# Kernel optimization log

Hardware: AMD Instinct MI355X
Metric: run time of the kernel (lower is better)

The kernel has to match this reference:

```python
import jax, jax.numpy as jnp
import numpy as np

HEADS = 16
HD = 64
LN_EPS = 1e-5


def swish(x):
    return x * jax.nn.sigmoid(x)


def layer_norm(x):
    mu = jnp.mean(x, axis=-1, keepdims=True)
    var = jnp.var(x, axis=-1, keepdims=True)
    return (x - mu) * jax.lax.rsqrt(var + LN_EPS)


def setup_inputs() -> dict:
    key = jax.random.key(0)
    ks = jax.random.split(key, 5)
    B, L, D = 4, 2048, 1024
    x = jax.random.normal(ks[0], (B, L, D), dtype=jnp.float32)
    W_fc = jax.random.normal(ks[1], (D, HEADS * HD * 3), dtype=jnp.float32) * (1.0 / np.sqrt(D))
    b_fc = jax.random.normal(ks[2], (HEADS * HD * 3,), dtype=jnp.float32) * 0.01
    W_fc2 = jax.random.normal(ks[3], (HEADS * HD, D), dtype=jnp.float32) * (1.0 / np.sqrt(HEADS * HD))
    b_fc2 = jax.random.normal(ks[4], (D,), dtype=jnp.float32) * 0.01
    return {"x": x, "W_fc": W_fc, "b_fc": b_fc, "W_fc2": W_fc2, "b_fc2": b_fc2}


def reference(x, W_fc, b_fc, W_fc2, b_fc2):
    B, L, D = x.shape
    # fused QKV projection with swish activation (dropout is identity in eval)
    qkv = swish(jnp.einsum('bld,de->ble', x, W_fc) + b_fc)
    qkv = qkv.reshape(B, L, HEADS, 3 * HD)
    q, k, v = jnp.split(qkv, 3, axis=-1)  # each [B, L, H, hd]
    # NOTE: original scales by sqrt(length), not sqrt(hd)
    scores = jnp.einsum('bwhd,bmhd->bhwm', q, k) / jnp.sqrt(jnp.float32(L))
    att = jax.nn.softmax(scores, axis=-1)  # [B, H, L, L]
    new_v = jnp.einsum('bhwm,bmhd->bwhd', att, v).reshape(B, L, HEADS * HD)
    m = swish(jnp.einsum('ble,ed->bld', new_v, W_fc2) + b_fc2)
    return layer_norm(x + m)
```

## Files before the change

### kernel.cpp

```cpp
#include <hip/hip_runtime.h>
#include <cstddef>
#include <cstdint>

typedef unsigned short u16;
typedef __attribute__((ext_vector_type(8))) short short8;
typedef __attribute__((ext_vector_type(4))) float floatx4;

#define C1_SCALE 0.031882111f
#define LOG2E    1.4426950408889634f

__device__ __forceinline__ u16 f2bf(float f) {
    union { float f; unsigned int i; } v; v.f = f;
    unsigned int b = v.i;
    b += 0x7FFFu + ((b >> 16) & 1u);
    return (u16)(b >> 16);
}

__device__ __forceinline__ unsigned pk2bf(float lo, float hi) {
#if __has_builtin(__builtin_amdgcn_cvt_pk_bf16_f32)
    auto v = __builtin_amdgcn_cvt_pk_bf16_f32(lo, hi);
    union { decltype(v) b; unsigned u; } c; c.b = v; return c.u;
#else
    return (unsigned)f2bf(lo) | ((unsigned)f2bf(hi) << 16);
#endif
}
__device__ __forceinline__ int4 pack8bf(float4 a, float4 b) {
    union { unsigned u[4]; int4 v; } c;
    c.u[0] = pk2bf(a.x, a.y); c.u[1] = pk2bf(a.z, a.w);
    c.u[2] = pk2bf(b.x, b.y); c.u[3] = pk2bf(b.z, b.w);
    return c.v;
}
__device__ __forceinline__ float fastrcp(float x) {
#if __has_builtin(__builtin_amdgcn_rcpf)
    return __builtin_amdgcn_rcpf(x);
#else
    return 1.0f / x;
#endif
}
__device__ __forceinline__ float swishf(float s) {
    float e = __builtin_amdgcn_exp2f(-s * LOG2E);
    return s * fastrcp(1.0f + e);
}
__device__ __forceinline__ void glds16(const void* g, void* l) {
    __builtin_amdgcn_global_load_lds(
        (const __attribute__((address_space(1))) void*)g,
        (__attribute__((address_space(3))) void*)l, 16, 0, 0);
}

__global__ __launch_bounds__(256) void cast_kernel(
    const float* __restrict__ x, u16* __restrict__ xb)
{
    const size_t i = ((size_t)blockIdx.x * 256 + threadIdx.x) * 8;
    float4 a = *(const float4*)&x[i];
    float4 b = *(const float4*)&x[i + 4];
    *(int4*)&xb[i] = pack8bf(a, b);
}

__global__ __launch_bounds__(256) void transpose_kernel(
    const float* __restrict__ src, u16* __restrict__ dst, int R, int C)
{
    __shared__ u16 t[32][33];
    const int tx = threadIdx.x & 31, ty = threadIdx.x >> 5;
    const int r0 = blockIdx.y * 32, c0 = blockIdx.x * 32;
#pragma unroll
    for (int i = 0; i < 4; ++i)
        t[ty + i * 8][tx] = f2bf(src[(size_t)(r0 + ty + i * 8) * C + c0 + tx]);
    __syncthreads();
#pragma unroll
    for (int i = 0; i < 4; ++i)
        dst[(size_t)(c0 + ty + i * 8) * R + r0 + tx] = t[tx][ty + i * 8];
}

#define GEMM_STAGE(AP, BP, Kdim)                                              \
    {                                                                          \
        _Pragma("unroll")                                                      \
        for (int i = 0; i < 4; ++i) {                                          \
            const int row = i * 32 + (tid >> 3);                               \
            const int gp  = (tid & 7) ^ (row & 7);                             \
            glds16(&AP[(size_t)(row0 + row) * Kdim + k0 + gp * 8],             \
                   &As[i * 32 + wid * 8][0]);                                  \
            glds16(&BP[(size_t)(col0 + row) * Kdim + k0 + gp * 8],             \
                   &Bs[i * 32 + wid * 8][0]);                                  \
        }                                                                      \
    }

#define GEMM_COMPUTE()                                                         \
    {                                                                          \
        _Pragma("unroll")                                                      \
        for (int kc = 0; kc < 2; ++kc) {                                       \
            short8 af[4], bf[4];                                               \
            const int gl = ((kc * 4 + quad) ^ (l16 & 7)) * 8;                  \
            _Pragma("unroll")                                                  \
            for (int mt = 0; mt < 4; ++mt)                                     \
                af[mt] = *(const short8*)&As[wm * 64 + mt * 16 + l16][gl];     \
            _Pragma("unroll")                                                  \
            for (int nt = 0; nt < 4; ++nt)                                     \
                bf[nt] = *(const short8*)&Bs[wn * 64 + nt * 16 + l16][gl];     \
            _Pragma("unroll")                                                  \
            for (int mt = 0; mt < 4; ++mt)                                     \
                _Pragma("unroll")                                              \
                for (int nt = 0; nt < 4; ++nt)                                 \
                    acc[mt][nt] = __builtin_amdgcn_mfma_f32_16x16x32_bf16(     \
                        af[mt], bf[nt], acc[mt][nt], 0, 0, 0);                 \
        }                                                                      \
    }

__global__ __launch_bounds__(256) void gemm_qkv_kernel(
    const u16* __restrict__ A, const u16* __restrict__ BT,
    const float* __restrict__ bias, u16* __restrict__ qk, u16* __restrict__ vT)
{
    const int K = 1024;
    const int tid  = threadIdx.x;
    const int wid  = tid >> 6;
    const int lane = tid & 63;
    const int quad = lane >> 4;
    const int l16  = lane & 15;
    const int wm = wid >> 1, wn = wid & 1;
    const int row0 = blockIdx.y * 128, col0 = blockIdx.x * 128;

    __shared__ __align__(16) u16 As[128][64];
    __shared__ __align__(16) u16 Bs[128][64];

    floatx4 acc[4][4] = {};

    for (int k0 = 0; k0 < K; k0 += 64) {
        if (k0) __syncthreads();
        GEMM_STAGE(A, BT, K);
        __syncthreads();
        GEMM_COMPUTE();
    }

    float bb[4];
#pragma unroll
    for (int nt = 0; nt < 4; ++nt)
        bb[nt] = bias[col0 + wn * 64 + nt * 16 + l16];

    const int b = row0 >> 11;
#pragma unroll
    for (int mt = 0; mt < 4; ++mt) {
        const int rbase = row0 + wm * 64 + mt * 16 + quad * 4;
        const int l0 = rbase & 2047;
#pragma unroll
        for (int nt = 0; nt < 4; ++nt) {
            const int c = col0 + wn * 64 + nt * 16 + l16;
            const unsigned h = (unsigned)c / 192u;
            const int w = c - (int)h * 192;
            float sw[4];
#pragma unroll
            for (int r = 0; r < 4; ++r)
                sw[r] = swishf(acc[mt][nt][r] + bb[nt]);
            if (w < 128) {
                const float scl = (w >= 64) ? C1_SCALE : 1.0f;
#pragma unroll
                for (int r = 0; r < 4; ++r)
                    qk[(size_t)(rbase + r) * 2048 + h * 128 + w] = f2bf(sw[r] * scl);
            } else {
                union { unsigned u[2]; uint2 v; } pk;
                pk.u[0] = pk2bf(sw[0], sw[1]);
                pk.u[1] = pk2bf(sw[2], sw[3]);
                *(uint2*)&vT[(size_t)((b * 16 + (int)h) * 64 + (w - 128)) * 2048 + l0] = pk.v;
            }
        }
    }
}

__global__ __launch_bounds__(256) void gemm_out_kernel(
    const u16* __restrict__ A, const u16* __restrict__ BT,
    const float* __restrict__ bias, const float* __restrict__ xres,
    float* __restrict__ out)
{
    const int K = 1024, N = 1024;
    const int tid  = threadIdx.x;
    const int wid  = tid >> 6;
    const int lane = tid & 63;
    const int quad = lane >> 4;
    const int l16  = lane & 15;
    const int wm = wid >> 1, wn = wid & 1;
    const int row0 = blockIdx.y * 128, col0 = blockIdx.x * 128;

    __shared__ __align__(16) u16 As[128][64];
    __shared__ __align__(16) u16 Bs[128][64];

    floatx4 acc[4][4] = {};

    for (int k0 = 0; k0 < K; k0 += 64) {
        if (k0) __syncthreads();
        GEMM_STAGE(A, BT, K);
        __syncthreads();
        GEMM_COMPUTE();
    }

    float bb[4];
#pragma unroll
    for (int nt = 0; nt < 4; ++nt)
        bb[nt] = bias[col0 + wn * 64 + nt * 16 + l16];

#pragma unroll
    for (int mt = 0; mt < 4; ++mt) {
#pragma unroll
        for (int nt = 0; nt < 4; ++nt) {
#pragma unroll
            for (int r = 0; r < 4; ++r) {
                int row = row0 + wm * 64 + mt * 16 + quad * 4 + r;
                int col = col0 + wn * 64 + nt * 16 + l16;
                float sw = swishf(acc[mt][nt][r] + bb[nt]);
                out[(size_t)row * N + col] = xres[(size_t)row * N + col] + sw;
            }
        }
    }
}

__global__ __launch_bounds__(256) void attn_kernel(
    const u16* __restrict__ qk, const u16* __restrict__ vT,
    u16* __restrict__ newv)
{
    const int tid  = threadIdx.x;
    const int wid  = tid >> 6;
    const int lane = tid & 63;
    const int quad = lane >> 4;
    const int l16  = lane & 15;
    const int id = blockIdx.x;
    const int qt = id >> 6;
    const int hb = id & 63;
    const int h  = hb & 15;
    const int b  = hb >> 4;

    const u16* qkb = qk + (size_t)b * 2048 * 2048;
    const u16* vTb = vT + (size_t)(b * 16 + h) * 64 * 2048;

    short8 qf[2][2];
#pragma unroll
    for (int it = 0; it < 2; ++it) {
        const int qrow = qt * 128 + (wid * 2 + it) * 16 + l16;
        const u16* qp = &qkb[(size_t)qrow * 2048 + h * 128];
        qf[it][0] = *(const short8*)&qp[quad * 8];
        qf[it][1] = *(const short8*)&qp[32 + quad * 8];
    }

    const short one = (short)0x3F80;
    const short8 ones = {one, one, one, one, one, one, one, one};

    __shared__ __align__(16) u16 Ks[2][64][64];
    __shared__ __align__(16) u16 Vt[2][64][64];
    __shared__ __align__(16) u16 Ps[4][16][64];

    const int srow = tid >> 3;
    const int sg0  = (tid & 7) ^ (srow & 7);
    floatx4 oacc[2][4] = {};
    floatx4 sumacc[2] = {};

#pragma unroll
    for (int i = 0; i < 2; ++i) {
        const int row = i * 32 + srow;
        glds16(&qkb[(size_t)row * 2048 + h * 128 + 64 + sg0 * 8],
               &Ks[0][i * 32 + wid * 8][0]);
        glds16(&vTb[(size_t)row * 2048 + sg0 * 8],
               &Vt[0][i * 32 + wid * 8][0]);
    }

    for (int kt = 0; kt < 32; ++kt) {
        const int cur = kt & 1;
        __syncthreads();

        if (kt + 1 < 32) {
            const int k0n = (kt + 1) * 64;
#pragma unroll
            for (int i = 0; i < 2; ++i) {
                const int row = i * 32 + srow;
                glds16(&qkb[(size_t)(k0n + row) * 2048 + h * 128 + 64 + sg0 * 8],
                       &Ks[cur ^ 1][i * 32 + wid * 8][0]);
                glds16(&vTb[(size_t)row * 2048 + k0n + sg0 * 8],
                       &Vt[cur ^ 1][i * 32 + wid * 8][0]);
            }
        }

        floatx4 sacc[2][4] = {};
#pragma unroll
        for (int kc = 0; kc < 2; ++kc) {
            const int gl = ((kc * 4 + quad) ^ (l16 & 7)) * 8;
#pragma unroll
            for (int nt = 0; nt < 4; ++nt) {
                short8 kf = *(const short8*)&Ks[cur][nt * 16 + l16][gl];
                sacc[0][nt] = __builtin_amdgcn_mfma_f32_16x16x32_bf16(kf, qf[0][kc], sacc[0][nt], 0, 0, 0);
                sacc[1][nt] = __builtin_amdgcn_mfma_f32_16x16x32_bf16(kf, qf[1][kc], sacc[1][nt], 0, 0, 0);
            }
        }

#pragma unroll
        for (int it = 0; it < 2; ++it) {
#pragma unroll
            for (int nt = 0; nt < 4; ++nt) {
                float p0 = __builtin_amdgcn_exp2f(sacc[it][nt][0]);
                float p1 = __builtin_amdgcn_exp2f(sacc[it][nt][1]);
                float p2 = __builtin_amdgcn_exp2f(sacc[it][nt][2]);
                float p3 = __builtin_amdgcn_exp2f(sacc[it][nt][3]);
                union { unsigned u[2]; uint2 v; } pk;
                pk.u[0] = pk2bf(p0, p1);
                pk.u[1] = pk2bf(p2, p3);
                const int col = (((nt * 2 + (quad >> 1)) ^ (l16 & 7)) * 8) + (quad & 1) * 4;
                *(uint2*)&Ps[wid][l16][col] = pk.v;
            }
#pragma unroll
            for (int kc = 0; kc < 2; ++kc) {
                const int gl = ((kc * 4 + quad) ^ (l16 & 7)) * 8;
                short8 pf = *(const short8*)&Ps[wid][l16][gl];
                sumacc[it] = __builtin_amdgcn_mfma_f32_16x16x32_bf16(ones, pf, sumacc[it], 0, 0, 0);
#pragma unroll
                for (int nt = 0; nt < 4; ++nt) {
                    short8 vf = *(const short8*)&Vt[cur][nt * 16 + l16][gl];
                    oacc[it][nt] = __builtin_amdgcn_mfma_f32_16x16x32_bf16(vf, pf, oacc[it][nt], 0, 0, 0);
                }
            }
        }
    }

#pragma unroll
    for (int it = 0; it < 2; ++it) {
        const float inv = fastrcp(sumacc[it][0]);
        const int row = qt * 128 + (wid * 2 + it) * 16 + l16;
        u16* orow = &newv[((size_t)b * 2048 + row) * 1024 + h * 64];
#pragma unroll
        for (int nt = 0; nt < 4; ++nt) {
            union { unsigned u[2]; uint2 v; } pk;
            pk.u[0] = pk2bf(oacc[it][nt][0] * inv, oacc[it][nt][1] * inv);
            pk.u[1] = pk2bf(oacc[it][nt][2] * inv, oacc[it][nt][3] * inv);
            *(uint2*)&orow[nt * 16 + quad * 4] = pk.v;
        }
    }
}

__global__ __launch_bounds__(256) void ln_kernel(
    const float* __restrict__ y, float* __restrict__ out)
{
    const int row = blockIdx.x;
    const int tid = threadIdx.x;
    const float* yr = y + (size_t)row * 1024;
    float v[4];
    float s1 = 0.f, s2 = 0.f;
#pragma unroll
    for (int i = 0; i < 4; ++i) {
        v[i] = yr[tid + i * 256];
        s1 += v[i];
        s2 += v[i] * v[i];
    }
#pragma unroll
    for (int off = 1; off < 64; off <<= 1) {
        s1 += __shfl_xor(s1, off, 64);
        s2 += __shfl_xor(s2, off, 64);
    }
    __shared__ float red1[4], red2[4];
    const int wid = tid >> 6, lane = tid & 63;
    if (lane == 0) { red1[wid] = s1; red2[wid] = s2; }
    __syncthreads();
    s1 = red1[0] + red1[1] + red1[2] + red1[3];
    s2 = red2[0] + red2[1] + red2[2] + red2[3];
    const float mu   = s1 * (1.0f / 1024.0f);
    const float var  = s2 * (1.0f / 1024.0f) - mu * mu;
    const float rstd = rsqrtf(var + 1e-5f);
    float* orow = out + (size_t)row * 1024;
#pragma unroll
    for (int i = 0; i < 4; ++i)
        orow[tid + i * 256] = (v[i] - mu) * rstd;
}

extern "C" void kernel_launch(void* const* d_in, const int* in_sizes, int n_in,
                              void* d_out, int out_size, void* d_ws, size_t ws_size,
                              hipStream_t stream) {
    const float* x     = (const float*)d_in[0];
    const float* W_fc  = (const float*)d_in[1];
    const float* b_fc  = (const float*)d_in[2];
    const float* W_fc2 = (const float*)d_in[3];
    const float* b_fc2 = (const float*)d_in[4];
    float* out = (float*)d_out;

    char* ob = (char*)d_out;
    u16* WfcT  = (u16*)ob;
    u16* Wfc2T = (u16*)(ob + 6291456);
    u16* xbf   = (u16*)(ob + 8388608);
    u16* newv  = (u16*)(ob + 8388608);

    char* ws = (char*)d_ws;
    u16*   qk = (u16*)ws;
    u16*   vT = (u16*)(ws + 33554432);
    float* y  = (float*)ws;

    cast_kernel<<<dim3(4096), 256, 0, stream>>>(x, xbf);
    transpose_kernel<<<dim3(96, 32), 256, 0, stream>>>(W_fc, WfcT, 1024, 3072);
    transpose_kernel<<<dim3(32, 32), 256, 0, stream>>>(W_fc2, Wfc2T, 1024, 1024);

    gemm_qkv_kernel<<<dim3(24, 64), 256, 0, stream>>>(xbf, WfcT, b_fc, qk, vT);

    attn_kernel<<<dim3(1024), 256, 0, stream>>>(qk, vT, newv);

    gemm_out_kernel<<<dim3(8, 64), 256, 0, stream>>>(newv, Wfc2T, b_fc2, x, y);

    ln_kernel<<<dim3(8192), 256, 0, stream>>>(y, out);
}
```

Measured before the change: 317.8 us.

## Merge prep kernels and switch attention to single-buffered 128-key tiles

The cast kernel and the two weight-transpose kernels are merged into one prep_kernel launch, with block ranges assigned to each job, to remove launch overhead. In the attention kernel the double-buffered 64-key K/V tiles are replaced by a single 128-key buffer that is loaded and then consumed in two 64-key halves. This halves the number of loop iterations and barriers, but the loads are no longer overlapped with compute inside a block and each block must wait for its loads before starting work.

New measurement: 308.8 us. 1.03x faster.

```diff
diff --git a/kernel.cpp b/kernel.cpp
--- a/kernel.cpp
+++ b/kernel.cpp
@@ -47,21 +47,30 @@
         (__attribute__((address_space(3))) void*)l, 16, 0, 0);
 }
 
-__global__ __launch_bounds__(256) void cast_kernel(
-    const float* __restrict__ x, u16* __restrict__ xb)
+__global__ __launch_bounds__(256) void prep_kernel(
+    const float* __restrict__ x,     u16* __restrict__ xb,
+    const float* __restrict__ W_fc,  u16* __restrict__ WfcT,
+    const float* __restrict__ W_fc2, u16* __restrict__ Wfc2T)
 {
-    const size_t i = ((size_t)blockIdx.x * 256 + threadIdx.x) * 8;
-    float4 a = *(const float4*)&x[i];
-    float4 b = *(const float4*)&x[i + 4];
-    *(int4*)&xb[i] = pack8bf(a, b);
-}
-
-__global__ __launch_bounds__(256) void transpose_kernel(
-    const float* __restrict__ src, u16* __restrict__ dst, int R, int C)
-{
+    const int id = blockIdx.x;
+    if (id < 4096) {
+        const size_t i = ((size_t)id * 256 + threadIdx.x) * 8;
+        float4 a = *(const float4*)&x[i];
+        float4 b = *(const float4*)&x[i + 4];
+        *(int4*)&xb[i] = pack8bf(a, b);
+        return;
+    }
     __shared__ u16 t[32][33];
+    const float* src; u16* dst; int R, C, bx, by;
+    if (id < 7168) {
+        const int w = id - 4096;
+        bx = w % 96; by = w / 96; src = W_fc; dst = WfcT; R = 1024; C = 3072;
+    } else {
+        const int w = id - 7168;
+        bx = w % 32; by = w / 32; src = W_fc2; dst = Wfc2T; R = 1024; C = 1024;
+    }
     const int tx = threadIdx.x & 31, ty = threadIdx.x >> 5;
-    const int r0 = blockIdx.y * 32, c0 = blockIdx.x * 32;
+    const int r0 = by * 32, c0 = bx * 32;
 #pragma unroll
     for (int i = 0; i < 4; ++i)
         t[ty + i * 8][tx] = f2bf(src[(size_t)(r0 + ty + i * 8) * C + c0 + tx]);
@@ -240,75 +249,70 @@
     const short one = (short)0x3F80;
     const short8 ones = {one, one, one, one, one, one, one, one};
 
-    __shared__ __align__(16) u16 Ks[2][64][64];
-    __shared__ __align__(16) u16 Vt[2][64][64];
+    __shared__ __align__(16) u16 Ks[128][64];
+    __shared__ __align__(16) u16 Vt[64][128];
     __shared__ __align__(16) u16 Ps[4][16][64];
 
-    const int srow = tid >> 3;
-    const int sg0  = (tid & 7) ^ (srow & 7);
+    const int krow_l = tid >> 3;
+    const int kgp    = (tid & 7) ^ (krow_l & 7);
+    const int vrow_l = tid >> 4;
+    const int vg     = tid & 15;
+    const int vgp    = ((vg >> 3) << 3) | ((vg & 7) ^ (vrow_l & 7));
+
     floatx4 oacc[2][4] = {};
     floatx4 sumacc[2] = {};
 
-#pragma unroll
-    for (int i = 0; i < 2; ++i) {
-        const int row = i * 32 + srow;
-        glds16(&qkb[(size_t)row * 2048 + h * 128 + 64 + sg0 * 8],
-               &Ks[0][i * 32 + wid * 8][0]);
-        glds16(&vTb[(size_t)row * 2048 + sg0 * 8],
-               &Vt[0][i * 32 + wid * 8][0]);
-    }
-
-    for (int kt = 0; kt < 32; ++kt) {
-        const int cur = kt & 1;
+    for (int kt = 0; kt < 16; ++kt) {
+        const int k0 = kt * 128;
+        if (kt) __syncthreads();
+#pragma unroll
+        for (int c = 0; c < 4; ++c)
+            glds16(&qkb[(size_t)(k0 + c * 32 + krow_l) * 2048 + h * 128 + 64 + kgp * 8],
+                   &Ks[c * 32 + wid * 8][0]);
+#pragma unroll
+        for (int c = 0; c < 4; ++c)
+            glds16(&vTb[(size_t)(c * 16 + vrow_l) * 2048 + k0 + vgp * 8],
+                   &Vt[c * 16 + wid * 4][0]);
         __syncthreads();
 
-        if (kt + 1 < 32) {
-            const int k0n = (kt + 1) * 64;
-#pragma unroll
-            for (int i = 0; i < 2; ++i) {
-                const int row = i * 32 + srow;
-                glds16(&qkb[(size_t)(k0n + row) * 2048 + h * 128 + 64 + sg0 * 8],
-                       &Ks[cur ^ 1][i * 32 + wid * 8][0]);
-                glds16(&vTb[(size_t)row * 2048 + k0n + sg0 * 8],
-                       &Vt[cur ^ 1][i * 32 + wid * 8][0]);
-            }
-        }
-
-        floatx4 sacc[2][4] = {};
-#pragma unroll
-        for (int kc = 0; kc < 2; ++kc) {
-            const int gl = ((kc * 4 + quad) ^ (l16 & 7)) * 8;
-#pragma unroll
-            for (int nt = 0; nt < 4; ++nt) {
-                short8 kf = *(const short8*)&Ks[cur][nt * 16 + l16][gl];
-                sacc[0][nt] = __builtin_amdgcn_mfma_f32_16x16x32_bf16(kf, qf[0][kc], sacc[0][nt], 0, 0, 0);
-                sacc[1][nt] = __builtin_amdgcn_mfma_f32_16x16x32_bf16(kf, qf[1][kc], sacc[1][nt], 0, 0, 0);
-            }
-        }
-
-#pragma unroll
-        for (int it = 0; it < 2; ++it) {
-#pragma unroll
-            for (int nt = 0; nt < 4; ++nt) {
-                float p0 = __builtin_amdgcn_exp2f(sacc[it][nt][0]);
-                float p1 = __builtin_amdgcn_exp2f(sacc[it][nt][1]);
-                float p2 = __builtin_amdgcn_exp2f(sacc[it][nt][2]);
-                float p3 = __builtin_amdgcn_exp2f(sacc[it][nt][3]);
-                union { unsigned u[2]; uint2 v; } pk;
-                pk.u[0] = pk2bf(p0, p1);
-                pk.u[1] = pk2bf(p2, p3);
-                const int col = (((nt * 2 + (quad >> 1)) ^ (l16 & 7)) * 8) + (quad & 1) * 4;
-                *(uint2*)&Ps[wid][l16][col] = pk.v;
-            }
+#pragma unroll
+        for (int s = 0; s < 2; ++s) {
+            floatx4 sacc[2][4] = {};
 #pragma unroll
             for (int kc = 0; kc < 2; ++kc) {
                 const int gl = ((kc * 4 + quad) ^ (l16 & 7)) * 8;
-                short8 pf = *(const short8*)&Ps[wid][l16][gl];
-                sumacc[it] = __builtin_amdgcn_mfma_f32_16x16x32_bf16(ones, pf, sumacc[it], 0, 0, 0);
 #pragma unroll
                 for (int nt = 0; nt < 4; ++nt) {
-                    short8 vf = *(const short8*)&Vt[cur][nt * 16 + l16][gl];
-                    oacc[it][nt] = __builtin_amdgcn_mfma_f32_16x16x32_bf16(vf, pf, oacc[it][nt], 0, 0, 0);
+                    short8 kf = *(const short8*)&Ks[s * 64 + nt * 16 + l16][gl];
+                    sacc[0][nt] = __builtin_amdgcn_mfma_f32_16x16x32_bf16(kf, qf[0][kc], sacc[0][nt], 0, 0, 0);
+                    sacc[1][nt] = __builtin_amdgcn_mfma_f32_16x16x32_bf16(kf, qf[1][kc], sacc[1][nt], 0, 0, 0);
+                }
+            }
+
+#pragma unroll
+            for (int it = 0; it < 2; ++it) {
+#pragma unroll
+                for (int nt = 0; nt < 4; ++nt) {
+                    float p0 = __builtin_amdgcn_exp2f(sacc[it][nt][0]);
+                    float p1 = __builtin_amdgcn_exp2f(sacc[it][nt][1]);
+                    float p2 = __builtin_amdgcn_exp2f(sacc[it][nt][2]);
+                    float p3 = __builtin_amdgcn_exp2f(sacc[it][nt][3]);
+                    union { unsigned u[2]; uint2 v; } pk;
+                    pk.u[0] = pk2bf(p0, p1);
+                    pk.u[1] = pk2bf(p2, p3);
+                    const int col = (((nt * 2 + (quad >> 1)) ^ (l16 & 7)) * 8) + (quad & 1) * 4;
+                    *(uint2*)&Ps[wid][l16][col] = pk.v;
+                }
+#pragma unroll
+                for (int kc = 0; kc < 2; ++kc) {
+                    const int gl = ((kc * 4 + quad) ^ (l16 & 7)) * 8;
+                    short8 pf = *(const short8*)&Ps[wid][l16][gl];
+                    sumacc[it] = __builtin_amdgcn_mfma_f32_16x16x32_bf16(ones, pf, sumacc[it], 0, 0, 0);
+#pragma unroll
+                    for (int nt = 0; nt < 4; ++nt) {
+                        short8 vf = *(const short8*)&Vt[nt * 16 + l16][s * 64 + gl];
+                        oacc[it][nt] = __builtin_amdgcn_mfma_f32_16x16x32_bf16(vf, pf, oacc[it][nt], 0, 0, 0);
+                    }
                 }
             }
         }
@@ -384,9 +388,7 @@
     u16*   vT = (u16*)(ws + 33554432);
     float* y  = (float*)ws;
 
-    cast_kernel<<<dim3(4096), 256, 0, stream>>>(x, xbf);
-    transpose_kernel<<<dim3(96, 32), 256, 0, stream>>>(W_fc, WfcT, 1024, 3072);
-    transpose_kernel<<<dim3(32, 32), 256, 0, stream>>>(W_fc2, Wfc2T, 1024, 1024);
+    prep_kernel<<<dim3(8192), 256, 0, stream>>>(x, xbf, W_fc, WfcT, W_fc2, Wfc2T);
 
     gemm_qkv_kernel<<<dim3(24, 64), 256, 0, stream>>>(xbf, WfcT, b_fc, qk, vT);
 
```
